# Kernel optimization log

Measured on AMD Instinct MI355X. Metric: run time of the kernel, lower is better.

The kernel has to match this reference:

```python
import jax, jax.numpy as jnp
import numpy as np

B, H, W = 64, 512, 512          # batch, image height/width
BH, BW = 8, 8                   # block_size
K = 256                         # n_blocks (codebook size)
L = BH * BW                     # block_len = 64
HT, WT = H // BH, W // BW       # tiles per axis
T = HT * WT                     # tiles_per_img = 4096
BETA = 35.0


def _unfold(img):
    # img: (B, 1, H, W) -> patches (B, T, L), matching torch.nn.Unfold
    # with kernel=stride=(BH,BW): tiles row-major, patch flattened (kh, kw).
    x = img.reshape(B, 1, HT, BH, WT, BW)
    x = x.transpose(0, 2, 4, 1, 3, 5)          # (B, HT, WT, 1, BH, BW)
    return x.reshape(B, T, L)


def _fold(patches):
    # patches: (B, T, L) -> img (B, 1, H, W); exact inverse of _unfold
    # (non-overlapping, so Fold is pure reassembly, no accumulation).
    x = patches.reshape(B, HT, WT, 1, BH, BW)
    x = x.transpose(0, 3, 1, 4, 2, 5)          # (B, 1, HT, BH, WT, BW)
    return x.reshape(B, 1, H, W)


def setup_inputs() -> dict:
    key = jax.random.key(0)
    k1, k2 = jax.random.split(key)
    target_img = jax.random.uniform(k1, (B, 1, H, W), dtype=jnp.float32)
    # Learned codebook parameter (Haar-ish init in the original; values
    # don't change the math being tested).
    blocks = jax.random.uniform(k2, (K, BH, BW), dtype=jnp.float32)
    return {"target_img": target_img, "blocks": blocks}


def reference(target_img, blocks):
    patches = _unfold(target_img).reshape(B * T, L)   # (N, L), N = B*T
    codes = blocks.reshape(K, L)                      # (K, L)

    # Squared distances ||a - b||^2 via the expanded form to avoid
    # materializing the (N, K, L) difference tensor.
    a2 = jnp.sum(patches * patches, axis=-1, keepdims=True)   # (N, 1)
    b2 = jnp.sum(codes * codes, axis=-1)                      # (K,)
    ab = patches @ codes.T                                    # (N, K)
    sqerr = a2 - 2.0 * ab + b2                                # (N, K)

    block_weights = jax.nn.softmax(-BETA * sqerr, axis=-1)    # (N, K)
    uf_reconstructed = block_weights @ codes                  # (N, L)

    reconstructed = _fold(uf_reconstructed.reshape(B, T, L))  # (B,1,H,W)
    choice_penalty = jnp.mean(
        jnp.minimum(block_weights, 1.0 - block_weights)) * K
    return reconstructed, choice_penalty
```

## Files before the change

### kernel.cpp

```cpp
#include <hip/hip_runtime.h>


typedef short short8 __attribute__((ext_vector_type(8)));
typedef float floatx4 __attribute__((ext_vector_type(4)));

namespace {
constexpr float BETA_C = 35.0f;
constexpr float TAU    = 1e-6f;
constexpr float INV_N  = 1.0f / 262144.0f;
constexpr size_t IMG_ELEMS = (size_t)64 * 512 * 512;
constexpr int WB = 0;
constexpr int WR = 0;
constexpr int NWORDS = 8192;
}

__device__ __forceinline__ unsigned short f2bf(float x) {
  unsigned u = __float_as_uint(x);
  return (unsigned short)((u + 0x7FFFu + ((u >> 16) & 1u)) >> 16);
}
__device__ __forceinline__ float bf2f(unsigned short h) {
  return __uint_as_float((unsigned)h << 16);
}
__device__ __forceinline__ unsigned pack2(unsigned short lo, unsigned short hi) {
  return (unsigned)lo | ((unsigned)hi << 16);
}
__device__ __forceinline__ void cvt8(float4 a, float4 b, short8& h, short8& l) {
  float f[8] = {a.x, a.y, a.z, a.w, b.x, b.y, b.z, b.w};
#pragma unroll
  for (int i = 0; i < 8; ++i) {
    unsigned short hh = f2bf(f[i]);
    h[i] = (short)hh;
    l[i] = (short)f2bf(f[i] - bf2f(hh));
  }
}

__global__ void pack_codes(const float* __restrict__ blk,
                           unsigned* __restrict__ wsBh,
                           unsigned* __restrict__ wsBl,
                           float* __restrict__ wsB2) {
  const int c = threadIdx.x;
  const float* src = blk + c * 64;
  float b2 = 0.f;
#pragma unroll
  for (int g = 0; g < 8; ++g) {
#pragma unroll
    for (int t = 0; t < 4; ++t) {
      float v0 = src[g * 8 + 2 * t], v1 = src[g * 8 + 2 * t + 1];
      b2 += v0 * v0 + v1 * v1;
      unsigned short h0 = f2bf(v0), h1 = f2bf(v1);
      unsigned short l0 = f2bf(v0 - bf2f(h0)), l1 = f2bf(v1 - bf2f(h1));
      wsBh[(c * 8 + g) * 4 + t] = pack2(h0, h1);
      wsBl[(c * 8 + g) * 4 + t] = pack2(l0, l1);
    }
  }
  wsB2[c] = b2;
}

__global__ __launch_bounds__(256, 4) void recon_kernel(
    const float* __restrict__ img, const float* __restrict__ blk,
    const unsigned* __restrict__ wsBh, const unsigned* __restrict__ wsBl,
    const float* __restrict__ wsB2, float* __restrict__ out,
    float* __restrict__ penAcc) {
  __shared__ unsigned sMem[NWORDS];
  float* sMemF = reinterpret_cast<float*>(sMem);

  const int tid = threadIdx.x;
  const int lane = tid & 63;
  const int wave = tid >> 6;
  const int b = blockIdx.x >> 6;
  const int ht = blockIdx.x & 63;
  const int c15 = lane & 15;
  const int q = lane >> 4;

  const float* imgBase = img + (size_t)b * (512 * 512) + (size_t)(ht * 8) * 512;
  const float* aptr = imgBase + q * 512 + (wave * 16 + c15) * 8;
  float4 v00 = *reinterpret_cast<const float4*>(aptr);
  float4 v01 = *reinterpret_cast<const float4*>(aptr + 4);
  float4 v10 = *reinterpret_cast<const float4*>(aptr + 2048);
  float4 v11 = *reinterpret_cast<const float4*>(aptr + 2048 + 4);

  {
    const uint4* src = reinterpret_cast<const uint4*>(wsBh);
#pragma unroll
    for (int i = 0; i < 8; ++i) {
      int j = i * 256 + tid;
      int sj = (j & ~7) | ((j ^ (j >> 3)) & 7);
      *reinterpret_cast<uint4*>(&sMem[WB + j * 4]) = src[sj];
    }
  }

  short8 ah[2], al[2];
  cvt8(v00, v01, ah[0], al[0]);
  cvt8(v10, v11, ah[1], al[1]);
  __syncthreads();

  floatx4 acc[16];
#pragma unroll
  for (int n = 0; n < 16; ++n) acc[n] = (floatx4){0.f, 0.f, 0.f, 0.f};

  const int kx = c15 & 7;
  const unsigned* pb0 = &sMem[WB + (8 * c15 + (q ^ kx)) * 4];
  const unsigned* pb1 = &sMem[WB + (8 * c15 + ((q ^ 4) ^ kx)) * 4];

#pragma unroll
  for (int n = 0; n < 16; ++n) {
    short8 b0 = *reinterpret_cast<const short8*>(pb0 + 512 * n);
    short8 b1 = *reinterpret_cast<const short8*>(pb1 + 512 * n);
    acc[n] = __builtin_amdgcn_mfma_f32_16x16x32_bf16(ah[0], b0, acc[n], 0, 0, 0);
    acc[n] = __builtin_amdgcn_mfma_f32_16x16x32_bf16(al[0], b0, acc[n], 0, 0, 0);
    acc[n] = __builtin_amdgcn_mfma_f32_16x16x32_bf16(ah[1], b1, acc[n], 0, 0, 0);
    acc[n] = __builtin_amdgcn_mfma_f32_16x16x32_bf16(al[1], b1, acc[n], 0, 0, 0);
  }
  __syncthreads();
  {
    const uint4* src = reinterpret_cast<const uint4*>(wsBl);
#pragma unroll
    for (int i = 0; i < 8; ++i) {
      int j = i * 256 + tid;
      int sj = (j & ~7) | ((j ^ (j >> 3)) & 7);
      *reinterpret_cast<uint4*>(&sMem[WB + j * 4]) = src[sj];
    }
  }
  __syncthreads();
#pragma unroll
  for (int n = 0; n < 16; ++n) {
    short8 b0 = *reinterpret_cast<const short8*>(pb0 + 512 * n);
    short8 b1 = *reinterpret_cast<const short8*>(pb1 + 512 * n);
    acc[n] = __builtin_amdgcn_mfma_f32_16x16x32_bf16(ah[0], b0, acc[n], 0, 0, 0);
    acc[n] = __builtin_amdgcn_mfma_f32_16x16x32_bf16(al[0], b0, acc[n], 0, 0, 0);
    acc[n] = __builtin_amdgcn_mfma_f32_16x16x32_bf16(ah[1], b1, acc[n], 0, 0, 0);
    acc[n] = __builtin_amdgcn_mfma_f32_16x16x32_bf16(al[1], b1, acc[n], 0, 0, 0);
  }

#pragma unroll
  for (int n = 0; n < 16; ++n) {
    float b2v = wsB2[16 * n + c15];
#pragma unroll
    for (int r = 0; r < 4; ++r)
      acc[n][r] = fmaf(2.0f * BETA_C, acc[n][r], -BETA_C * b2v);
  }
  float mx[4], sm[4];
#pragma unroll
  for (int r = 0; r < 4; ++r) {
    float m = acc[0][r];
#pragma unroll
    for (int n = 1; n < 16; ++n) m = fmaxf(m, acc[n][r]);
#pragma unroll
    for (int off = 1; off <= 8; off <<= 1) m = fmaxf(m, __shfl_xor(m, off, 64));
    mx[r] = m;
    sm[r] = 0.f;
  }
#pragma unroll
  for (int n = 0; n < 16; ++n)
#pragma unroll
    for (int r = 0; r < 4; ++r) {
      acc[n][r] = __expf(acc[n][r] - mx[r]);
      sm[r] += acc[n][r];
    }
#pragma unroll
  for (int r = 0; r < 4; ++r) {
#pragma unroll
    for (int off = 1; off <= 8; off <<= 1) sm[r] += __shfl_xor(sm[r], off, 64);
    sm[r] = 1.0f / sm[r];
  }

  float pen = 0.f;
  float rr[16] = {0.f, 0.f, 0.f, 0.f, 0.f, 0.f, 0.f, 0.f,
                  0.f, 0.f, 0.f, 0.f, 0.f, 0.f, 0.f, 0.f};
#pragma unroll
  for (int r = 0; r < 4; ++r) {
#pragma unroll
    for (int n = 0; n < 16; ++n) {
      float w = acc[n][r] * sm[r];
      pen += fminf(w, 1.0f - w);
      unsigned long long m = __ballot(w > TAU);
      while (m) {
        int L = __builtin_ctzll(m);
        m &= m - 1;
        float wL = __uint_as_float(
            __builtin_amdgcn_readlane(__float_as_uint(w), L));
        float v = wL * blk[(16 * n + (L & 15)) * 64 + lane];
        switch (L >> 4) {
          case 0: rr[r] += v; break;
          case 1: rr[4 + r] += v; break;
          case 2: rr[8 + r] += v; break;
          case 3: rr[12 + r] += v; break;
        }
      }
    }
  }
#pragma unroll
  for (int off = 1; off <= 32; off <<= 1) pen += __shfl_xor(pen, off, 64);
  if (lane == 0) atomicAdd(penAcc, pen);

  __syncthreads();

#pragma unroll
  for (int pl = 0; pl < 16; ++pl)
    sMemF[WR + (wave * 16 + pl) * 68 + lane] = rr[pl];
  float* outBase = out + (size_t)b * (512 * 512) + (size_t)(ht * 8) * 512 +
                   wave * 128;
#pragma unroll
  for (int i = 0; i < 4; ++i) {
    int f = i * 64 + lane;
    int row = f >> 5;
    int cc = f & 31;
    int wtl = cc >> 1, hw = cc & 1;
    float4 v = *reinterpret_cast<const float4*>(
        &sMemF[WR + (wave * 16 + wtl) * 68 + row * 8 + hw * 4]);
    *reinterpret_cast<float4*>(outBase + row * 512 + cc * 4) = v;
  }
}

__global__ void finalize_kernel(float* penSlot) {
  *penSlot = (*penSlot) * INV_N;
}

extern "C" void kernel_launch(void* const* d_in, const int* in_sizes, int n_in,
                              void* d_out, int out_size, void* d_ws, size_t ws_size,
                              hipStream_t stream) {
  const float* img = (const float*)d_in[0];
  const float* blk = (const float*)d_in[1];
  float* out = (float*)d_out;
  float* penSlot = out + IMG_ELEMS;

  unsigned* wsBh = (unsigned*)d_ws;
  unsigned* wsBl = wsBh + 8192;
  float* wsB2 = (float*)(wsBl + 8192);

  pack_codes<<<dim3(1), dim3(256), 0, stream>>>(blk, wsBh, wsBl, wsB2);
  hipMemsetAsync(penSlot, 0, sizeof(float), stream);
  recon_kernel<<<dim3(4096), dim3(256), 0, stream>>>(img, blk, wsBh, wsBl,
                                                     wsB2, out, penSlot);
  finalize_kernel<<<dim3(1), dim3(1), 0, stream>>>(penSlot);
}
```

Measured before the change: 328.4 us.

## Split codebook in halves with online softmax and closed-form penalty

Processes the 256 codes in two halves of 128 using an online softmax: a running max and sum, with the reconstruction accumulators rescaled when the max changes. This halves the shared-memory footprint, allowing five blocks per CU, and prefetches the next codebook tile into registers while MFMAs run. The choice penalty is now computed exactly in closed form from the max weight (1/sum) rather than per-element min operations. Normalisation is deferred to the output store, the low×low correction MFMAs for the low codebook part are dropped, and the finalize kernel is folded into the atomic. Risks are slightly lower precision in the distance computation and extra rescale shuffles.

New measurement: 382.3 us. 16.4% more time.

```diff
diff --git a/kernel.cpp b/kernel.cpp
--- a/kernel.cpp
+++ b/kernel.cpp
@@ -9,9 +9,9 @@
 constexpr float TAU    = 1e-6f;
 constexpr float INV_N  = 1.0f / 262144.0f;
 constexpr size_t IMG_ELEMS = (size_t)64 * 512 * 512;
-constexpr int WB = 0;
 constexpr int WR = 0;
-constexpr int NWORDS = 8192;
+constexpr int WS = 4352;
+constexpr int NWORDS = 4416;
 }
 
 __device__ __forceinline__ unsigned short f2bf(float x) {
@@ -24,14 +24,18 @@
 __device__ __forceinline__ unsigned pack2(unsigned short lo, unsigned short hi) {
   return (unsigned)lo | ((unsigned)hi << 16);
 }
-__device__ __forceinline__ void cvt8(float4 a, float4 b, short8& h, short8& l) {
+__device__ __forceinline__ void cvt8t(float4 a, float4 b, short8& h, short8& l) {
   float f[8] = {a.x, a.y, a.z, a.w, b.x, b.y, b.z, b.w};
 #pragma unroll
   for (int i = 0; i < 8; ++i) {
     unsigned short hh = f2bf(f[i]);
     h[i] = (short)hh;
-    l[i] = (short)f2bf(f[i] - bf2f(hh));
-  }
+    float lf = f[i] - bf2f(hh);
+    l[i] = (short)(__float_as_uint(lf) >> 16);
+  }
+}
+__device__ __forceinline__ int swz(int j) {
+  return (j & ~7) | ((j ^ (j >> 3)) & 7);
 }
 
 __global__ void pack_codes(const float* __restrict__ blk,
@@ -56,13 +60,14 @@
   wsB2[c] = b2;
 }
 
-__global__ __launch_bounds__(256, 4) void recon_kernel(
+__global__ __launch_bounds__(256, 5) void recon_kernel(
     const float* __restrict__ img, const float* __restrict__ blk,
     const unsigned* __restrict__ wsBh, const unsigned* __restrict__ wsBl,
     const float* __restrict__ wsB2, float* __restrict__ out,
     float* __restrict__ penAcc) {
   __shared__ unsigned sMem[NWORDS];
   float* sMemF = reinterpret_cast<float*>(sMem);
+  uint4* sMem4 = reinterpret_cast<uint4*>(sMem);
 
   const int tid = threadIdx.x;
   const int lane = tid & 63;
@@ -79,119 +84,150 @@
   float4 v10 = *reinterpret_cast<const float4*>(aptr + 2048);
   float4 v11 = *reinterpret_cast<const float4*>(aptr + 2048 + 4);
 
+  uint4 tH[4], tL[4];
   {
     const uint4* src = reinterpret_cast<const uint4*>(wsBh);
 #pragma unroll
-    for (int i = 0; i < 8; ++i) {
-      int j = i * 256 + tid;
-      int sj = (j & ~7) | ((j ^ (j >> 3)) & 7);
-      *reinterpret_cast<uint4*>(&sMem[WB + j * 4]) = src[sj];
-    }
+    for (int i = 0; i < 4; ++i) tH[i] = src[swz(i * 256 + tid)];
   }
 
   short8 ah[2], al[2];
-  cvt8(v00, v01, ah[0], al[0]);
-  cvt8(v10, v11, ah[1], al[1]);
-  __syncthreads();
-
-  floatx4 acc[16];
-#pragma unroll
-  for (int n = 0; n < 16; ++n) acc[n] = (floatx4){0.f, 0.f, 0.f, 0.f};
+  cvt8t(v00, v01, ah[0], al[0]);
+  cvt8t(v10, v11, ah[1], al[1]);
 
   const int kx = c15 & 7;
-  const unsigned* pb0 = &sMem[WB + (8 * c15 + (q ^ kx)) * 4];
-  const unsigned* pb1 = &sMem[WB + (8 * c15 + ((q ^ 4) ^ kx)) * 4];
-
-#pragma unroll
-  for (int n = 0; n < 16; ++n) {
-    short8 b0 = *reinterpret_cast<const short8*>(pb0 + 512 * n);
-    short8 b1 = *reinterpret_cast<const short8*>(pb1 + 512 * n);
-    acc[n] = __builtin_amdgcn_mfma_f32_16x16x32_bf16(ah[0], b0, acc[n], 0, 0, 0);
-    acc[n] = __builtin_amdgcn_mfma_f32_16x16x32_bf16(al[0], b0, acc[n], 0, 0, 0);
-    acc[n] = __builtin_amdgcn_mfma_f32_16x16x32_bf16(ah[1], b1, acc[n], 0, 0, 0);
-    acc[n] = __builtin_amdgcn_mfma_f32_16x16x32_bf16(al[1], b1, acc[n], 0, 0, 0);
-  }
-  __syncthreads();
-  {
-    const uint4* src = reinterpret_cast<const uint4*>(wsBl);
-#pragma unroll
-    for (int i = 0; i < 8; ++i) {
-      int j = i * 256 + tid;
-      int sj = (j & ~7) | ((j ^ (j >> 3)) & 7);
-      *reinterpret_cast<uint4*>(&sMem[WB + j * 4]) = src[sj];
-    }
-  }
-  __syncthreads();
-#pragma unroll
-  for (int n = 0; n < 16; ++n) {
-    short8 b0 = *reinterpret_cast<const short8*>(pb0 + 512 * n);
-    short8 b1 = *reinterpret_cast<const short8*>(pb1 + 512 * n);
-    acc[n] = __builtin_amdgcn_mfma_f32_16x16x32_bf16(ah[0], b0, acc[n], 0, 0, 0);
-    acc[n] = __builtin_amdgcn_mfma_f32_16x16x32_bf16(al[0], b0, acc[n], 0, 0, 0);
-    acc[n] = __builtin_amdgcn_mfma_f32_16x16x32_bf16(ah[1], b1, acc[n], 0, 0, 0);
-    acc[n] = __builtin_amdgcn_mfma_f32_16x16x32_bf16(al[1], b1, acc[n], 0, 0, 0);
-  }
-
-#pragma unroll
-  for (int n = 0; n < 16; ++n) {
-    float b2v = wsB2[16 * n + c15];
-#pragma unroll
-    for (int r = 0; r < 4; ++r)
-      acc[n][r] = fmaf(2.0f * BETA_C, acc[n][r], -BETA_C * b2v);
-  }
-  float mx[4], sm[4];
-#pragma unroll
-  for (int r = 0; r < 4; ++r) {
-    float m = acc[0][r];
-#pragma unroll
-    for (int n = 1; n < 16; ++n) m = fmaxf(m, acc[n][r]);
-#pragma unroll
-    for (int off = 1; off <= 8; off <<= 1) m = fmaxf(m, __shfl_xor(m, off, 64));
-    mx[r] = m;
-    sm[r] = 0.f;
-  }
-#pragma unroll
-  for (int n = 0; n < 16; ++n)
-#pragma unroll
-    for (int r = 0; r < 4; ++r) {
-      acc[n][r] = __expf(acc[n][r] - mx[r]);
-      sm[r] += acc[n][r];
-    }
-#pragma unroll
-  for (int r = 0; r < 4; ++r) {
-#pragma unroll
-    for (int off = 1; off <= 8; off <<= 1) sm[r] += __shfl_xor(sm[r], off, 64);
-    sm[r] = 1.0f / sm[r];
-  }
-
-  float pen = 0.f;
+  const unsigned* pb0 = &sMem[(8 * c15 + (q ^ kx)) * 4];
+  const unsigned* pb1 = &sMem[(8 * c15 + ((q ^ 4) ^ kx)) * 4];
+
+  float m[4], sm[4];
   float rr[16] = {0.f, 0.f, 0.f, 0.f, 0.f, 0.f, 0.f, 0.f,
                   0.f, 0.f, 0.f, 0.f, 0.f, 0.f, 0.f, 0.f};
-#pragma unroll
-  for (int r = 0; r < 4; ++r) {
-#pragma unroll
-    for (int n = 0; n < 16; ++n) {
-      float w = acc[n][r] * sm[r];
-      pen += fminf(w, 1.0f - w);
-      unsigned long long m = __ballot(w > TAU);
-      while (m) {
-        int L = __builtin_ctzll(m);
-        m &= m - 1;
-        float wL = __uint_as_float(
-            __builtin_amdgcn_readlane(__float_as_uint(w), L));
-        float v = wL * blk[(16 * n + (L & 15)) * 64 + lane];
+
+#pragma unroll
+  for (int h = 0; h < 2; ++h) {
+    if (h == 1) __syncthreads();
+#pragma unroll
+    for (int i = 0; i < 4; ++i) sMem4[i * 256 + tid] = tH[i];
+    __syncthreads();
+    {
+      const uint4* src = reinterpret_cast<const uint4*>(wsBl) + h * 1024;
+#pragma unroll
+      for (int i = 0; i < 4; ++i) tL[i] = src[swz(i * 256 + tid)];
+    }
+    floatx4 acc[8];
+#pragma unroll
+    for (int n = 0; n < 8; ++n) acc[n] = (floatx4){0.f, 0.f, 0.f, 0.f};
+#pragma unroll
+    for (int n = 0; n < 8; ++n) {
+      short8 b0 = *reinterpret_cast<const short8*>(pb0 + 512 * n);
+      short8 b1 = *reinterpret_cast<const short8*>(pb1 + 512 * n);
+      acc[n] = __builtin_amdgcn_mfma_f32_16x16x32_bf16(ah[0], b0, acc[n], 0, 0, 0);
+      acc[n] = __builtin_amdgcn_mfma_f32_16x16x32_bf16(al[0], b0, acc[n], 0, 0, 0);
+      acc[n] = __builtin_amdgcn_mfma_f32_16x16x32_bf16(ah[1], b1, acc[n], 0, 0, 0);
+      acc[n] = __builtin_amdgcn_mfma_f32_16x16x32_bf16(al[1], b1, acc[n], 0, 0, 0);
+    }
+    __syncthreads();
+#pragma unroll
+    for (int i = 0; i < 4; ++i) sMem4[i * 256 + tid] = tL[i];
+    __syncthreads();
+    if (h == 0) {
+      const uint4* src = reinterpret_cast<const uint4*>(wsBh) + 1024;
+#pragma unroll
+      for (int i = 0; i < 4; ++i) tH[i] = src[swz(i * 256 + tid)];
+    }
+#pragma unroll
+    for (int n = 0; n < 8; ++n) {
+      short8 b0 = *reinterpret_cast<const short8*>(pb0 + 512 * n);
+      short8 b1 = *reinterpret_cast<const short8*>(pb1 + 512 * n);
+      acc[n] = __builtin_amdgcn_mfma_f32_16x16x32_bf16(ah[0], b0, acc[n], 0, 0, 0);
+      acc[n] = __builtin_amdgcn_mfma_f32_16x16x32_bf16(ah[1], b1, acc[n], 0, 0, 0);
+    }
+
+#pragma unroll
+    for (int n = 0; n < 8; ++n) {
+      float b2v = wsB2[128 * h + 16 * n + c15];
+#pragma unroll
+      for (int r = 0; r < 4; ++r)
+        acc[n][r] = fmaf(2.0f * BETA_C, acc[n][r], -BETA_C * b2v);
+    }
+    float M[4];
+#pragma unroll
+    for (int r = 0; r < 4; ++r) {
+      float mm = acc[0][r];
+#pragma unroll
+      for (int n = 1; n < 8; ++n) mm = fmaxf(mm, acc[n][r]);
+#pragma unroll
+      for (int off = 1; off <= 8; off <<= 1) mm = fmaxf(mm, __shfl_xor(mm, off, 64));
+      M[r] = mm;
+    }
+    if (h == 0) {
+#pragma unroll
+      for (int r = 0; r < 4; ++r) { m[r] = M[r]; sm[r] = 0.f; }
+    } else {
+      float scl[4];
+#pragma unroll
+      for (int r = 0; r < 4; ++r) {
+        float mn = fmaxf(m[r], M[r]);
+        scl[r] = __expf(m[r] - mn);
+        m[r] = mn;
+        sm[r] *= scl[r];
+      }
+#pragma unroll
+      for (int qq = 0; qq < 4; ++qq)
+#pragma unroll
+        for (int r = 0; r < 4; ++r) {
+          float sq = __shfl(scl[r], qq * 16 + c15, 64);
+          rr[4 * qq + r] *= sq;
+        }
+    }
+#pragma unroll
+    for (int n = 0; n < 8; ++n)
+#pragma unroll
+      for (int r = 0; r < 4; ++r) {
+        float e = __expf(acc[n][r] - m[r]);
+        acc[n][r] = e;
+        sm[r] += e;
+      }
+#pragma unroll
+    for (int n = 0; n < 8; ++n) {
+      float em = fmaxf(fmaxf(acc[n][0], acc[n][1]), fmaxf(acc[n][2], acc[n][3]));
+      unsigned long long msk = __ballot(em > TAU);
+      while (msk) {
+        int L = __builtin_ctzll(msk);
+        msk &= msk - 1;
+        float w0 = __uint_as_float(__builtin_amdgcn_readlane(__float_as_uint(acc[n][0]), L));
+        float w1 = __uint_as_float(__builtin_amdgcn_readlane(__float_as_uint(acc[n][1]), L));
+        float w2 = __uint_as_float(__builtin_amdgcn_readlane(__float_as_uint(acc[n][2]), L));
+        float w3 = __uint_as_float(__builtin_amdgcn_readlane(__float_as_uint(acc[n][3]), L));
+        float bv = blk[(size_t)(128 * h + 16 * n + (L & 15)) * 64 + lane];
         switch (L >> 4) {
-          case 0: rr[r] += v; break;
-          case 1: rr[4 + r] += v; break;
-          case 2: rr[8 + r] += v; break;
-          case 3: rr[12 + r] += v; break;
+          case 0: rr[0] += w0 * bv;  rr[1] += w1 * bv;  rr[2] += w2 * bv;  rr[3] += w3 * bv;  break;
+          case 1: rr[4] += w0 * bv;  rr[5] += w1 * bv;  rr[6] += w2 * bv;  rr[7] += w3 * bv;  break;
+          case 2: rr[8] += w0 * bv;  rr[9] += w1 * bv;  rr[10] += w2 * bv; rr[11] += w3 * bv; break;
+          default: rr[12] += w0 * bv; rr[13] += w1 * bv; rr[14] += w2 * bv; rr[15] += w3 * bv; break;
         }
       }
     }
   }
-#pragma unroll
-  for (int off = 1; off <= 32; off <<= 1) pen += __shfl_xor(pen, off, 64);
-  if (lane == 0) atomicAdd(penAcc, pen);
+
+  float invS[4];
+#pragma unroll
+  for (int r = 0; r < 4; ++r) {
+#pragma unroll
+    for (int off = 1; off <= 8; off <<= 1) sm[r] += __shfl_xor(sm[r], off, 64);
+    invS[r] = 1.0f / sm[r];
+  }
+  float pen = 0.f;
+  if (c15 == 0) {
+#pragma unroll
+    for (int r = 0; r < 4; ++r) {
+      pen += (invS[r] > 0.5f) ? (2.0f - 2.0f * invS[r]) : 1.0f;
+      sMemF[WS + wave * 16 + 4 * q + r] = invS[r];
+    }
+  }
+  pen += __shfl_xor(pen, 16, 64);
+  pen += __shfl_xor(pen, 32, 64);
+  if (lane == 0) atomicAdd(penAcc, pen * INV_N);
 
   __syncthreads();
 
@@ -208,12 +244,10 @@
     int wtl = cc >> 1, hw = cc & 1;
     float4 v = *reinterpret_cast<const float4*>(
         &sMemF[WR + (wave * 16 + wtl) * 68 + row * 8 + hw * 4]);
+    float is = sMemF[WS + wave * 16 + wtl];
+    v.x *= is; v.y *= is; v.z *= is; v.w *= is;
     *reinterpret_cast<float4*>(outBase + row * 512 + cc * 4) = v;
   }
-}
-
-__global__ void finalize_kernel(float* penSlot) {
-  *penSlot = (*penSlot) * INV_N;
 }
 
 extern "C" void kernel_launch(void* const* d_in, const int* in_sizes, int n_in,
@@ -232,5 +266,4 @@
   hipMemsetAsync(penSlot, 0, sizeof(float), stream);
   recon_kernel<<<dim3(4096), dim3(256), 0, stream>>>(img, blk, wsBh, wsBl,
                                                      wsB2, out, penSlot);
-  finalize_kernel<<<dim3(1), dim3(1), 0, stream>>>(penSlot);
-}
+}
```
